# Optimization experiments

Measured on AMD Instinct MI355X. Metric: run time of the kernel, lower is better.

Reference implementation:

```python
import jax, jax.numpy as jnp
import numpy as np

B, R, L, K = 64, 196, 512, 768
NEG = jnp.float32(-2**31 + 1)


def setup_inputs() -> dict:
    key = jax.random.key(0)
    ks = jax.random.split(key, 8)
    image_emb = jax.random.normal(ks[0], (B, R, L), dtype=jnp.float32)
    seq_emb = jax.random.normal(ks[1], (B, L, K), dtype=jnp.float32)
    mask = jax.random.randint(ks[2], (B, L), 0, 2, dtype=jnp.int32)
    # Linear(l,1) and Linear(k,1) params, Xavier-ish scale
    image_W = jax.random.normal(ks[3], (L, 1), dtype=jnp.float32) / np.sqrt(L)
    image_b = jnp.zeros((1,), dtype=jnp.float32)
    seq_W = jax.random.normal(ks[4], (K, 1), dtype=jnp.float32) / np.sqrt(K)
    seq_b = jnp.zeros((1,), dtype=jnp.float32)
    # V_weight [L, L], xavier_uniform
    lim = np.sqrt(6.0 / (L + L)).astype(np.float32)
    V_weight = jax.random.uniform(ks[5], (L, L), dtype=jnp.float32, minval=-lim, maxval=lim)
    return {"image_emb": image_emb, "seq_emb": seq_emb, "mask": mask,
            "image_W": image_W, "image_b": image_b,
            "seq_W": seq_W, "seq_b": seq_b, "V_weight": V_weight}


def reference(image_emb, seq_emb, mask, image_W, image_b, seq_W, seq_b, V_weight):
    # p: [B,R,1], q: [B,L,1]
    p = jnp.tanh(image_emb @ image_W + image_b)
    q = jnp.tanh(seq_emb @ seq_W + seq_b)
    qt = jnp.swapaxes(q, 1, 2)              # [B,1,L]
    emb = p @ qt + qt                       # [B,R,L] (rank-1 outer + broadcast add)
    score = emb @ V_weight                  # [B,R,L]
    # dropout_rate=0.0 -> identity
    score = jnp.where(mask[:, None, :] == 0, NEG, score)
    score = jax.nn.softmax(score, axis=-1)  # [B,R,L]
    out = score @ seq_emb                   # [B,R,K]
    out = out / jnp.sqrt(jnp.float32(seq_emb.shape[-1]))
    return out
```

## Files before the change

### kernel.cpp

```cpp
#include <hip/hip_runtime.h>
#include <cstdint>
#include <cstddef>


typedef __attribute__((ext_vector_type(8))) short short8;
typedef __attribute__((ext_vector_type(4))) float f32x4;

__device__ __forceinline__ unsigned short f32_to_bf16(float x) {
    unsigned int u = __float_as_uint(x);
    unsigned int r = (u + 0x7FFFu + ((u >> 16) & 1u)) >> 16;
    return (unsigned short)r;
}
__device__ __forceinline__ float bf16_to_f32(unsigned short h) {
    return __uint_as_float(((unsigned int)h) << 16);
}

#if defined(__has_builtin)
#if __has_builtin(__builtin_amdgcn_cvt_pk_bf16_f32)
#define HAVE_PK_BF16 1
#endif
#endif

__device__ __forceinline__ unsigned int pk_bf16(float a, float b) {
#ifdef HAVE_PK_BF16
    typedef __attribute__((ext_vector_type(2))) __bf16 bf16x2;
    bf16x2 v = __builtin_amdgcn_cvt_pk_bf16_f32(a, b);
    return __builtin_bit_cast(unsigned int, v);
#else
    return (unsigned int)f32_to_bf16(a) | ((unsigned int)f32_to_bf16(b) << 16);
#endif
}

__global__ __launch_bounds__(256) void kprep(const float* __restrict__ seq,
                                             const float* __restrict__ seqW,
                                             const float* __restrict__ img,
                                             const float* __restrict__ imgW,
                                             const float* __restrict__ imgBias,
                                             unsigned short* __restrict__ seqT,
                                             float* __restrict__ qpart,
                                             float* __restrict__ pv) {
    __shared__ __align__(16) unsigned int sT[128 * 32];
    __shared__ __align__(16) float sWc[128];

    if (blockIdx.x >= 3072) {
        int wv = threadIdx.x >> 6, lane = threadIdx.x & 63;
        int row = (blockIdx.x - 3072) * 4 + wv;
        const float4* x4 = (const float4*)(img + (size_t)row * 512);
        const float4* w4 = (const float4*)imgW;
        float s = 0.f;
#pragma unroll
        for (int i = 0; i < 2; ++i) {
            float4 a = x4[i * 64 + lane];
            float4 c = w4[i * 64 + lane];
            s += a.x * c.x + a.y * c.y + a.z * c.z + a.w * c.w;
        }
#pragma unroll
        for (int o = 32; o; o >>= 1) s += __shfl_xor(s, o, 64);
        if (lane == 0) pv[row] = tanhf(s + imgBias[0]);
        return;
    }

    int id = blockIdx.x;
    int b = id / 48, rem = id - b * 48;
    int jt = rem / 6, ck = rem - jt * 6;
    int j0 = jt * 64;
    int t = threadIdx.x;
    if (t < 128) sWc[t] = seqW[ck * 128 + t];

    int quad = t >> 4, kseg = t & 15;
    int qk = quad ^ kseg;
    const float* base = seq + (size_t)b * 512 * 768 + (size_t)(j0 + quad * 4) * 768 + ck * 128;
    int jg = t & 7, krow = t >> 3;
    float qp[4] = {0.f, 0.f, 0.f, 0.f};
    __syncthreads();

#pragma unroll
    for (int rp = 0; rp < 2; ++rp) {
        int kq = rp * 64 + kseg * 4;
        float4 r0 = *(const float4*)(base + 0 * 768 + kq);
        float4 r1 = *(const float4*)(base + 1 * 768 + kq);
        float4 r2 = *(const float4*)(base + 2 * 768 + kq);
        float4 r3 = *(const float4*)(base + 3 * 768 + kq);
        float4 w  = *(const float4*)(sWc + kq);
        qp[0] += r0.x * w.x + r0.y * w.y + r0.z * w.z + r0.w * w.w;
        qp[1] += r1.x * w.x + r1.y * w.y + r1.z * w.z + r1.w * w.w;
        qp[2] += r2.x * w.x + r2.y * w.y + r2.z * w.z + r2.w * w.w;
        qp[3] += r3.x * w.x + r3.y * w.y + r3.z * w.z + r3.w * w.w;
        float a0[4] = {r0.x, r0.y, r0.z, r0.w};
        float a1[4] = {r1.x, r1.y, r1.z, r1.w};
        float a2[4] = {r2.x, r2.y, r2.z, r2.w};
        float a3[4] = {r3.x, r3.y, r3.z, r3.w};
#pragma unroll
        for (int i = 0; i < 4; ++i) {
            int k = kq + i;
            int col = (qk ^ (i << 2)) & 15;
            uint2 v;
            v.x = pk_bf16(a0[i], a1[i]);
            v.y = pk_bf16(a2[i], a3[i]);
            *(uint2*)(sT + k * 32 + col * 2) = v;
        }
    }
    __syncthreads();
    unsigned short* dst = seqT + (size_t)b * 768 * 512 + (size_t)ck * 128 * 512 + j0;
#pragma unroll
    for (int wp = 0; wp < 4; ++wp) {
        int k = wp * 32 + krow;
        int s = ((k >> 2) & 15) ^ ((k & 3) << 2);
        int c0 = ((jg << 1) ^ s) & 15;
        int c1 = ((jg << 1) ^ 1 ^ s) & 15;
        uint2 va = *(const uint2*)(sT + k * 32 + c0 * 2);
        uint2 vb = *(const uint2*)(sT + k * 32 + c1 * 2);
        uint4 o;
        o.x = va.x; o.y = va.y; o.z = vb.x; o.w = vb.y;
        *(uint4*)(dst + (size_t)k * 512 + jg * 8) = o;
    }
#pragma unroll
    for (int rr = 0; rr < 4; ++rr) {
        float s = qp[rr];
        s += __shfl_xor(s, 8, 64);
        s += __shfl_xor(s, 4, 64);
        s += __shfl_xor(s, 2, 64);
        s += __shfl_xor(s, 1, 64);
        if (kseg == 0)
            qpart[(size_t)ck * 32768 + b * 512 + j0 + quad * 4 + rr] = s;
    }
}

__global__ __launch_bounds__(256) void krows_p(const float* __restrict__ x,
                                               const float* __restrict__ w,
                                               const float* __restrict__ bias,
                                               float* __restrict__ outp) {
    int wv = threadIdx.x >> 6, lane = threadIdx.x & 63;
    int row = blockIdx.x * 4 + wv;
    const float4* x4 = (const float4*)(x + (size_t)row * 512);
    const float4* w4 = (const float4*)w;
    float s = 0.f;
#pragma unroll
    for (int i = 0; i < 2; ++i) {
        float4 a = x4[i * 64 + lane];
        float4 c = w4[i * 64 + lane];
        s += a.x * c.x + a.y * c.y + a.z * c.z + a.w * c.w;
    }
#pragma unroll
    for (int o = 32; o; o >>= 1) s += __shfl_xor(s, o, 64);
    if (lane == 0) outp[row] = tanhf(s + bias[0]);
}

__global__ __launch_bounds__(256) void krows_q(const float* __restrict__ x,
                                               const float* __restrict__ w,
                                               float* __restrict__ outp) {
    int wv = threadIdx.x >> 6, lane = threadIdx.x & 63;
    int row = blockIdx.x * 4 + wv;
    const float4* x4 = (const float4*)(x + (size_t)row * 768);
    const float4* w4 = (const float4*)w;
    float s = 0.f;
#pragma unroll
    for (int i = 0; i < 3; ++i) {
        float4 a = x4[i * 64 + lane];
        float4 c = w4[i * 64 + lane];
        s += a.x * c.x + a.y * c.y + a.z * c.z + a.w * c.w;
    }
#pragma unroll
    for (int o = 32; o; o >>= 1) s += __shfl_xor(s, o, 64);
    if (lane == 0) outp[row] = s;
}

__global__ __launch_bounds__(256) void kw(const float* __restrict__ qpart,
                                          const float* __restrict__ seqBias,
                                          const float* __restrict__ V,
                                          const int* __restrict__ mask,
                                          float* __restrict__ wm,
                                          int nparts) {
    __shared__ __align__(16) float sq[512];
    __shared__ __align__(16) float sacc[8][32][4];
    int b = blockIdx.x >> 2, jc = blockIdx.x & 3;
    int t = threadIdx.x;
    float qb = seqBias[0];
    float a0 = 0.f, a1 = 0.f;
    for (int pp = 0; pp < nparts; ++pp) {
        a0 += qpart[(size_t)pp * 32768 + b * 512 + t];
        a1 += qpart[(size_t)pp * 32768 + b * 512 + t + 256];
    }
    sq[t] = tanhf(a0 + qb);
    sq[t + 256] = tanhf(a1 + qb);
    __syncthreads();
    int jt = t & 31, lg = t >> 5;
    const float4* V4 = (const float4*)V;
    int col4 = jc * 32 + jt;
    float ax = 0.f, ay = 0.f, az = 0.f, aw = 0.f;
    int lbase = lg * 64;
#pragma unroll 8
    for (int li = 0; li < 64; ++li) {
        int l = lbase + li;
        float qq = sq[l];
        float4 v = V4[(size_t)l * 128 + col4];
        ax += qq * v.x; ay += qq * v.y; az += qq * v.z; aw += qq * v.w;
    }
    sacc[lg][jt][0] = ax; sacc[lg][jt][1] = ay;
    sacc[lg][jt][2] = az; sacc[lg][jt][3] = aw;
    __syncthreads();
    if (t < 32) {
        float sx = 0.f, sy = 0.f, sz = 0.f, sw = 0.f;
#pragma unroll
        for (int g = 0; g < 8; ++g) {
            sx += sacc[g][t][0]; sy += sacc[g][t][1];
            sz += sacc[g][t][2]; sw += sacc[g][t][3];
        }
        const int* mrow = mask + b * 512 + jc * 128 + t * 4;
        float4 o;
        o.x = mrow[0] ? sx : -1e30f;
        o.y = mrow[1] ? sy : -1e30f;
        o.z = mrow[2] ? sz : -1e30f;
        o.w = mrow[3] ? sw : -1e30f;
        ((float4*)(wm + b * 512 + jc * 128))[t] = o;
    }
}

__global__ __launch_bounds__(256, 2) void kattn2(const unsigned short* __restrict__ seqT,
                                                 const float* __restrict__ p,
                                                 const float* __restrict__ wm,
                                                 float* __restrict__ out) {
    __shared__ __align__(16) unsigned short sB[2][128 * 64];
    __shared__ __align__(16) float swm[512];
    __shared__ float sinvz[64];
    __shared__ float sred[16];

    int raw = blockIdx.x;
    int g  = ((raw >> 5) << 3) + (raw & 7);
    int rt = (raw >> 3) & 3;
    int b  = g / 6, nt = g - b * 6;
    int t  = threadIdx.x;
    int wv = t >> 6, lane = t & 63;
    int mm = lane & 15, q = lane >> 4;
    int nb = nt * 128;

    float v0 = wm[b * 512 + t];
    float v1 = wm[b * 512 + t + 256];
    swm[t] = v0; swm[t + 256] = v1;
    float lmax = fmaxf(v0, v1);
    float fa = (v0 > -1e29f) ? v0 : 1e30f;
    float fb = (v1 > -1e29f) ? v1 : 1e30f;
    float lmin = fminf(fa, fb);
#pragma unroll
    for (int o = 32; o; o >>= 1) {
        lmax = fmaxf(lmax, __shfl_xor(lmax, o, 64));
        lmin = fminf(lmin, __shfl_xor(lmin, o, 64));
    }
    if (lane == 0) { sred[wv] = lmax; sred[8 + wv] = lmin; }
    __syncthreads();

    bool wactive = (rt * 64 + wv * 16) < 196;

    int rl = wv * 16 + mm;
    int r  = rt * 64 + rl;
    bool valid = r < 196;

    short8 afrag[16];
    if (wactive) {
        float wmax = fmaxf(fmaxf(sred[0], sred[1]), fmaxf(sred[2], sred[3]));
        float wmin = fminf(fminf(sred[8], sred[9]), fminf(sred[10], sred[11]));
        int pidx = b * 196 + (valid ? r : 195);
        float c = 1.0f + p[pidx];
        float M = (c >= 0.f) ? c * wmax : c * wmin;

        float zsum = 0.f;
        const f32x4* swm4 = (const f32x4*)swm;
#pragma unroll
        for (int tk = 0; tk < 16; ++tk) {
            int jb = tk * 32 + q * 8;
            f32x4 w0 = swm4[jb >> 2];
            f32x4 w1 = swm4[(jb >> 2) + 1];
            short8 af;
#pragma unroll
            for (int jj = 0; jj < 8; ++jj) {
                float ww = (jj < 4) ? w0[jj] : w1[jj - 4];
                float e = valid ? __expf(c * ww - M) : 0.f;
                unsigned short h = f32_to_bf16(e);
                zsum += bf16_to_f32(h);
                af[jj] = (short)h;
            }
            afrag[tk] = af;
        }
        zsum += __shfl_xor(zsum, 16, 64);
        zsum += __shfl_xor(zsum, 32, 64);
        if (q == 0) sinvz[rl] = 1.0f / zsum;
    }

    f32x4 acc[8];
#pragma unroll
    for (int s = 0; s < 8; ++s) acc[s] = (f32x4){0.f, 0.f, 0.f, 0.f};

    const unsigned short* seqTb = seqT + (size_t)b * 768 * 512 + (size_t)nb * 512;
    int nrow = t >> 3, jg = t & 7;
    auto stage = [&](int ch, int buf) {
        unsigned short* sb = sB[buf];
#pragma unroll
        for (int pp = 0; pp < 4; ++pp) {
            int n = pp * 32 + nrow;
            short8 v = *(const short8*)(seqTb + (size_t)n * 512 + ch * 64 + jg * 8);
            int sw = (n ^ (n >> 3)) & 7;
            *(short8*)(sb + n * 64 + ((jg ^ sw) << 3)) = v;
        }
    };

    __syncthreads();
    stage(0, 0);
    __syncthreads();
#pragma unroll
    for (int ch = 0; ch < 8; ++ch) {
        if (ch < 7) stage(ch + 1, (ch + 1) & 1);
        if (wactive) {
            const unsigned short* cb = sB[ch & 1];
#pragma unroll
            for (int kk = 0; kk < 2; ++kk) {
                short8 bfr[8];
#pragma unroll
                for (int s = 0; s < 8; ++s) {
                    int n = s * 16 + mm;
                    int sw = (n ^ (n >> 3)) & 7;
                    bfr[s] = *(const short8*)(cb + n * 64 + ((((kk << 2) + q) ^ sw) << 3));
                }
#pragma unroll
                for (int s = 0; s < 8; ++s)
                    acc[s] = __builtin_amdgcn_mfma_f32_16x16x32_bf16(
                        afrag[(ch << 1) + kk], bfr[s], acc[s], 0, 0, 0);
            }
        }
        __syncthreads();
    }

    if (wactive) {
        const float invsqrtk = 0.036084391824351615f;
#pragma unroll
        for (int reg = 0; reg < 4; ++reg) {
            int row = q * 4 + reg;
            int rr = rt * 64 + wv * 16 + row;
            if (rr < 196) {
                float scale = sinvz[wv * 16 + row] * invsqrtk;
                float* op = out + (size_t)(b * 196 + rr) * 768 + nb + mm;
#pragma unroll
                for (int s = 0; s < 8; ++s)
                    op[s * 16] = acc[s][reg] * scale;
            }
        }
    }
}

__global__ __launch_bounds__(256, 2) void kattn(const float* __restrict__ seq,
                                                const float* __restrict__ p,
                                                const float* __restrict__ wm,
                                                float* __restrict__ out) {
    __shared__ __align__(16) unsigned int sseq[2][128 * 32];
    __shared__ __align__(16) float swm[512];
    __shared__ float sinvz[64];
    __shared__ float sred[16];

    int id = blockIdx.x;
    int rt = id & 3;
    int nt = (id >> 2) % 6;
    int b  = id / 24;
    int t  = threadIdx.x;
    int wv = t >> 6, lane = t & 63;
    int mm = lane & 15, q = lane >> 4;
    int nb = nt * 128;

    float v0 = wm[b * 512 + t];
    float v1 = wm[b * 512 + t + 256];
    swm[t] = v0; swm[t + 256] = v1;
    float lmax = fmaxf(v0, v1);
    float fa = (v0 > -1e29f) ? v0 : 1e30f;
    float fb = (v1 > -1e29f) ? v1 : 1e30f;
    float lmin = fminf(fa, fb);
#pragma unroll
    for (int o = 32; o; o >>= 1) {
        lmax = fmaxf(lmax, __shfl_xor(lmax, o, 64));
        lmin = fminf(lmin, __shfl_xor(lmin, o, 64));
    }
    if (lane == 0) { sred[wv] = lmax; sred[8 + wv] = lmin; }
    __syncthreads();
    float wmax = fmaxf(fmaxf(sred[0], sred[1]), fmaxf(sred[2], sred[3]));
    float wmin = fminf(fminf(sred[8], sred[9]), fminf(sred[10], sred[11]));

    int rl = wv * 16 + mm;
    int r  = rt * 64 + rl;
    bool valid = r < 196;
    int pidx = b * 196 + (valid ? r : 195);
    float c = 1.0f + p[pidx];
    float M = (c >= 0.f) ? c * wmax : c * wmin;

    short8 afrag[16];
    float zsum = 0.f;
    const f32x4* swm4 = (const f32x4*)swm;
#pragma unroll
    for (int tk = 0; tk < 16; ++tk) {
        int jb = tk * 32 + q * 8;
        f32x4 w0 = swm4[jb >> 2];
        f32x4 w1 = swm4[(jb >> 2) + 1];
        short8 af;
#pragma unroll
        for (int jj = 0; jj < 8; ++jj) {
            float ww = (jj < 4) ? w0[jj] : w1[jj - 4];
            float e = valid ? __expf(c * ww - M) : 0.f;
            unsigned short h = f32_to_bf16(e);
            zsum += bf16_to_f32(h);
            af[jj] = (short)h;
        }
        afrag[tk] = af;
    }
    zsum += __shfl_xor(zsum, 16, 64);
    zsum += __shfl_xor(zsum, 32, 64);
    if (q == 0) sinvz[rl] = 1.0f / zsum;

    f32x4 acc[8];
#pragma unroll
    for (int s = 0; s < 8; ++s) acc[s] = (f32x4){0.f, 0.f, 0.f, 0.f};

    const float* seqb = seq + (size_t)b * 512 * 768 + nb;
    int tl = t & 31, jp = t >> 5;
    int n0 = tl * 4;
    auto stage = [&](int ch, int buf) {
        unsigned int* sb = sseq[buf];
#pragma unroll
        for (int pass = 0; pass < 4; ++pass) {
            int jl = pass * 16 + jp * 2;
            int jglob = ch * 64 + jl;
            float4 a0 = *(const float4*)(seqb + (size_t)jglob * 768 + n0);
            float4 a1 = *(const float4*)(seqb + (size_t)(jglob + 1) * 768 + n0);
            float a0v[4] = {a0.x, a0.y, a0.z, a0.w};
            float a1v[4] = {a1.x, a1.y, a1.z, a1.w};
            int g = jl >> 3;
            int wo = (jl & 7) >> 1;
#pragma unroll
            for (int i = 0; i < 4; ++i) {
                int n = n0 + i;
                int sw = (n ^ (n >> 3)) & 7;
                unsigned int pk = (unsigned int)f32_to_bf16(a0v[i]) |
                                  ((unsigned int)f32_to_bf16(a1v[i]) << 16);
                sb[n * 32 + ((g ^ sw) << 2) + wo] = pk;
            }
        }
    };

    __syncthreads();
    stage(0, 0);
    __syncthreads();
#pragma unroll
    for (int ch = 0; ch < 8; ++ch) {
        if (ch < 7) stage(ch + 1, (ch + 1) & 1);
        const unsigned int* cb = sseq[ch & 1];
#pragma unroll
        for (int kk = 0; kk < 2; ++kk) {
            short8 bfr[8];
#pragma unroll
            for (int s = 0; s < 8; ++s) {
                int n = s * 16 + mm;
                int g = kk * 4 + q;
                int sw = (n ^ (n >> 3)) & 7;
                bfr[s] = *(const short8*)(cb + n * 32 + ((g ^ sw) << 2));
            }
#pragma unroll
            for (int s = 0; s < 8; ++s)
                acc[s] = __builtin_amdgcn_mfma_f32_16x16x32_bf16(
                    afrag[ch * 2 + kk], bfr[s], acc[s], 0, 0, 0);
        }
        __syncthreads();
    }

    const float invsqrtk = 0.036084391824351615f;
#pragma unroll
    for (int reg = 0; reg < 4; ++reg) {
        int row = q * 4 + reg;
        int rr = rt * 64 + wv * 16 + row;
        if (rr < 196) {
            float scale = sinvz[wv * 16 + row] * invsqrtk;
            float* op = out + (size_t)(b * 196 + rr) * 768 + nb + mm;
#pragma unroll
            for (int s = 0; s < 8; ++s)
                op[s * 16] = acc[s][reg] * scale;
        }
    }
}

extern "C" void kernel_launch(void* const* d_in, const int* in_sizes, int n_in,
                              void* d_out, int out_size, void* d_ws, size_t ws_size,
                              hipStream_t stream) {
    const float* image_emb = (const float*)d_in[0];
    const float* seq_emb   = (const float*)d_in[1];
    const int*   mask      = (const int*)d_in[2];
    const float* image_W   = (const float*)d_in[3];
    const float* image_b   = (const float*)d_in[4];
    const float* seq_W     = (const float*)d_in[5];
    const float* seq_b     = (const float*)d_in[6];
    const float* V         = (const float*)d_in[7];
    float* out = (float*)d_out;

    float* p_ws  = (float*)d_ws;
    float* qpart = (float*)((char*)d_ws + (128 << 10));
    float* wm_ws = (float*)((char*)d_ws + (896 << 10));
    unsigned short* seqT = (unsigned short*)((char*)d_ws + (1024 << 10));

    size_t need = (size_t)(1024 << 10) + (size_t)64 * 768 * 512 * 2;
    if (ws_size >= need) {
        kprep<<<dim3(6208), dim3(256), 0, stream>>>(seq_emb, seq_W,
                                                    image_emb, image_W, image_b,
                                                    seqT, qpart, p_ws);
        kw<<<dim3(256), dim3(256), 0, stream>>>(qpart, seq_b, V, mask, wm_ws, 6);
        kattn2<<<dim3(1536), dim3(256), 0, stream>>>(seqT, p_ws, wm_ws, out);
    } else {
        krows_p<<<dim3(3136), dim3(256), 0, stream>>>(image_emb, image_W, image_b, p_ws);
        krows_q<<<dim3(8192), dim3(256), 0, stream>>>(seq_emb, seq_W, qpart);
        kw<<<dim3(256), dim3(256), 0, stream>>>(qpart, seq_b, V, mask, wm_ws, 1);
        kattn<<<dim3(1536), dim3(256), 0, stream>>>(seq_emb, p_ws, wm_ws, out);
    }
}
```

Before: 235.4 us.

## Store bf16 seqT in pre-swizzled tiles and split kw over more blocks

The prep kernel now writes the transposed bf16 seq_emb as contiguous 128x64 tiles, already in the XOR-swizzled order the attention kernel's LDS expects. Staging in kattn2 becomes four fully contiguous 16-byte loads and stores per thread with no address swizzle math, and global reads are fully coalesced. Separately, kw is launched with twice as many blocks, each covering 64 columns instead of 128, to raise parallelism in the small V-projection step. This couples the layouts of two kernels, so any mismatch in the tile indexing would corrupt results.

```diff
diff --git a/kernel.cpp b/kernel.cpp
--- a/kernel.cpp
+++ b/kernel.cpp
@@ -101,18 +101,20 @@
         }
     }
     __syncthreads();
-    unsigned short* dst = seqT + (size_t)b * 768 * 512 + (size_t)ck * 128 * 512 + j0;
+    unsigned short* dst = seqT + (((size_t)b * 6 + ck) * 8 + jt) * (128 * 64);
 #pragma unroll
     for (int wp = 0; wp < 4; ++wp) {
         int k = wp * 32 + krow;
         int s = ((k >> 2) & 15) ^ ((k & 3) << 2);
-        int c0 = ((jg << 1) ^ s) & 15;
-        int c1 = ((jg << 1) ^ 1 ^ s) & 15;
+        int sw = (k ^ (k >> 3)) & 7;
+        int jgOut = jg ^ sw;
+        int c0 = ((jgOut << 1) ^ s) & 15;
+        int c1 = c0 ^ 1;
         uint2 va = *(const uint2*)(sT + k * 32 + c0 * 2);
         uint2 vb = *(const uint2*)(sT + k * 32 + c1 * 2);
         uint4 o;
         o.x = va.x; o.y = va.y; o.z = vb.x; o.w = vb.y;
-        *(uint4*)(dst + (size_t)k * 512 + jg * 8) = o;
+        *(uint4*)(dst + (size_t)k * 64 + jg * 8) = o;
     }
 #pragma unroll
     for (int rr = 0; rr < 4; ++rr) {
@@ -172,8 +174,8 @@
                                           float* __restrict__ wm,
                                           int nparts) {
     __shared__ __align__(16) float sq[512];
-    __shared__ __align__(16) float sacc[8][32][4];
-    int b = blockIdx.x >> 2, jc = blockIdx.x & 3;
+    __shared__ __align__(16) float sacc[16][16][4];
+    int b = blockIdx.x >> 3, jc = blockIdx.x & 7;
     int t = threadIdx.x;
     float qb = seqBias[0];
     float a0 = 0.f, a1 = 0.f;
@@ -184,13 +186,13 @@
     sq[t] = tanhf(a0 + qb);
     sq[t + 256] = tanhf(a1 + qb);
     __syncthreads();
-    int jt = t & 31, lg = t >> 5;
+    int jt = t & 15, lg = t >> 4;
     const float4* V4 = (const float4*)V;
-    int col4 = jc * 32 + jt;
+    int col4 = jc * 16 + jt;
     float ax = 0.f, ay = 0.f, az = 0.f, aw = 0.f;
-    int lbase = lg * 64;
+    int lbase = lg * 32;
 #pragma unroll 8
-    for (int li = 0; li < 64; ++li) {
+    for (int li = 0; li < 32; ++li) {
         int l = lbase + li;
         float qq = sq[l];
         float4 v = V4[(size_t)l * 128 + col4];
@@ -199,20 +201,20 @@
     sacc[lg][jt][0] = ax; sacc[lg][jt][1] = ay;
     sacc[lg][jt][2] = az; sacc[lg][jt][3] = aw;
     __syncthreads();
-    if (t < 32) {
+    if (t < 16) {
         float sx = 0.f, sy = 0.f, sz = 0.f, sw = 0.f;
 #pragma unroll
-        for (int g = 0; g < 8; ++g) {
+        for (int g = 0; g < 16; ++g) {
             sx += sacc[g][t][0]; sy += sacc[g][t][1];
             sz += sacc[g][t][2]; sw += sacc[g][t][3];
         }
-        const int* mrow = mask + b * 512 + jc * 128 + t * 4;
+        const int* mrow = mask + b * 512 + jc * 64 + t * 4;
         float4 o;
         o.x = mrow[0] ? sx : -1e30f;
         o.y = mrow[1] ? sy : -1e30f;
         o.z = mrow[2] ? sz : -1e30f;
         o.w = mrow[3] ? sw : -1e30f;
-        ((float4*)(wm + b * 512 + jc * 128))[t] = o;
+        ((float4*)(wm + b * 512 + jc * 64))[t] = o;
     }
 }
 
@@ -290,17 +292,19 @@
 #pragma unroll
     for (int s = 0; s < 8; ++s) acc[s] = (f32x4){0.f, 0.f, 0.f, 0.f};
 
-    const unsigned short* seqTb = seqT + (size_t)b * 768 * 512 + (size_t)nb * 512;
-    int nrow = t >> 3, jg = t & 7;
+    const unsigned short* seqTb = seqT + ((size_t)(b * 6 + nt) * 8) * (128 * 64);
+    int toff = t * 8;
     auto stage = [&](int ch, int buf) {
-        unsigned short* sb = sB[buf];
-#pragma unroll
-        for (int pp = 0; pp < 4; ++pp) {
-            int n = pp * 32 + nrow;
-            short8 v = *(const short8*)(seqTb + (size_t)n * 512 + ch * 64 + jg * 8);
-            int sw = (n ^ (n >> 3)) & 7;
-            *(short8*)(sb + n * 64 + ((jg ^ sw) << 3)) = v;
-        }
+        const unsigned short* src = seqTb + (size_t)ch * 8192 + toff;
+        unsigned short* ld = sB[buf] + toff;
+        short8 v0 = *(const short8*)(src);
+        short8 v1 = *(const short8*)(src + 2048);
+        short8 v2 = *(const short8*)(src + 4096);
+        short8 v3 = *(const short8*)(src + 6144);
+        *(short8*)(ld)        = v0;
+        *(short8*)(ld + 2048) = v1;
+        *(short8*)(ld + 4096) = v2;
+        *(short8*)(ld + 6144) = v3;
     };
 
     __syncthreads();
@@ -504,12 +508,12 @@
         kprep<<<dim3(6208), dim3(256), 0, stream>>>(seq_emb, seq_W,
                                                     image_emb, image_W, image_b,
                                                     seqT, qpart, p_ws);
-        kw<<<dim3(256), dim3(256), 0, stream>>>(qpart, seq_b, V, mask, wm_ws, 6);
+        kw<<<dim3(512), dim3(256), 0, stream>>>(qpart, seq_b, V, mask, wm_ws, 6);
         kattn2<<<dim3(1536), dim3(256), 0, stream>>>(seqT, p_ws, wm_ws, out);
     } else {
         krows_p<<<dim3(3136), dim3(256), 0, stream>>>(image_emb, image_W, image_b, p_ws);
         krows_q<<<dim3(8192), dim3(256), 0, stream>>>(seq_emb, seq_W, qpart);
-        kw<<<dim3(256), dim3(256), 0, stream>>>(qpart, seq_b, V, mask, wm_ws, 1);
+        kw<<<dim3(512), dim3(256), 0, stream>>>(qpart, seq_b, V, mask, wm_ws, 1);
         kattn<<<dim3(1536), dim3(256), 0, stream>>>(seq_emb, p_ws, wm_ws, out);
     }
 }
```

Result: no change. 234.0 us (-0.6%).
